# Kernel tuning notes

Measured on AMD Instinct MI355X. Metric: run time of the kernel, lower is better.

## Reference

```python
import jax, jax.numpy as jnp
import numpy as np

N = 50000      # nodes
E = 800000     # edges (before self loops)
IN = 128       # in_channels
C = 64         # out_channels per head
H = 4          # heads (both layers)
NEG_SLOPE = 0.2


def setup_inputs():
    key = jax.random.key(0)
    ks = jax.random.split(key, 14)
    nrm = lambda k, sh, s: jax.random.normal(k, sh, dtype=jnp.float32) * s
    x = nrm(ks[0], (N, IN), 1.0)
    edge_index = jax.random.randint(ks[1], (2, E), 0, N, dtype=jnp.int32)
    batch = jnp.zeros((N,), dtype=jnp.int32)
    edge_attr = jax.random.uniform(ks[2], (E, 1), dtype=jnp.float32)
    # layer 1 params (PyG GATConv: lin, att_src, att_dst, lin_edge, att_edge, bias)
    W1 = nrm(ks[3], (IN, H * C), 1.0 / np.sqrt(IN))
    We1 = nrm(ks[4], (1, H * C), 1.0)
    att_s1 = nrm(ks[5], (H, C), 1.0 / np.sqrt(C))
    att_d1 = nrm(ks[6], (H, C), 1.0 / np.sqrt(C))
    att_e1 = nrm(ks[7], (H, C), 1.0 / np.sqrt(C))
    b1 = jnp.zeros((H * C,), dtype=jnp.float32)
    # layer 2 params (in = H*C = 256)
    W2 = nrm(ks[8], (H * C, H * C), 1.0 / np.sqrt(H * C))
    We2 = nrm(ks[9], (1, H * C), 1.0)
    att_s2 = nrm(ks[10], (H, C), 1.0 / np.sqrt(C))
    att_d2 = nrm(ks[11], (H, C), 1.0 / np.sqrt(C))
    att_e2 = nrm(ks[12], (H, C), 1.0 / np.sqrt(C))
    b2 = jnp.zeros((H * C,), dtype=jnp.float32)
    return dict(x=x, edge_index=edge_index, batch=batch, edge_attr=edge_attr,
                W1=W1, We1=We1, att_s1=att_s1, att_d1=att_d1, att_e1=att_e1, b1=b1,
                W2=W2, We2=We2, att_s2=att_s2, att_d2=att_d2, att_e2=att_e2, b2=b2)


def gat_layer(h_in, src, dst, e_attr, W, We, att_s, att_d, att_e, b):
    n = h_in.shape[0]
    h = (h_in @ W).reshape(n, H, C)                      # [N,H,C]
    a_src = jnp.einsum('nhc,hc->nh', h, att_s)           # [N,H]
    a_dst = jnp.einsum('nhc,hc->nh', h, att_d)
    e = (e_attr @ We).reshape(-1, H, C)                  # [E',H,C]
    a_edge = jnp.einsum('ehc,hc->eh', e, att_e)          # [E',H]
    alpha = jax.nn.leaky_relu(a_src[src] + a_dst[dst] + a_edge, NEG_SLOPE)
    # softmax over edges grouped by destination node
    amax = jax.ops.segment_max(alpha, dst, num_segments=n)
    amax = jnp.where(jnp.isfinite(amax), amax, 0.0)
    ex = jnp.exp(alpha - amax[dst])
    denom = jax.ops.segment_sum(ex, dst, num_segments=n)
    a = ex / (denom[dst] + 1e-16)                        # [E',H]
    out = jax.ops.segment_sum(a[:, :, None] * h[src], dst, num_segments=n)
    return out.reshape(n, H * C) + b


def reference(x, edge_index, batch, edge_attr,
              W1, We1, att_s1, att_d1, att_e1, b1,
              W2, We2, att_s2, att_d2, att_e2, b2):
    n = x.shape[0]
    # PyG GATConv default: add self loops, self-loop edge_attr = mean fill
    loop = jnp.arange(n, dtype=edge_index.dtype)
    src = jnp.concatenate([edge_index[0], loop])
    dst = jnp.concatenate([edge_index[1], loop])
    ea_fill = jnp.broadcast_to(edge_attr.mean(axis=0, keepdims=True), (n, edge_attr.shape[1]))
    ea = jnp.concatenate([edge_attr, ea_fill], axis=0)
    h1 = gat_layer(x, src, dst, ea, W1, We1, att_s1, att_d1, att_e1, b1)
    h2 = gat_layer(h1, src, dst, ea, W2, We2, att_s2, att_d2, att_e2, b2)
    return h2
```

## Files before the change

### kernel.cpp

```cpp
#include <hip/hip_runtime.h>

#define NEG_SLOPE 0.2f

typedef __attribute__((ext_vector_type(8))) short bf16x8;
typedef __attribute__((ext_vector_type(4))) float f32x4;

__device__ inline unsigned short f2bf(float x) {
  unsigned int u = __float_as_uint(x);
  u += 0x7fffu + ((u >> 16) & 1u);
  return (unsigned short)(u >> 16);
}


__global__ void hist_kernel(const int* __restrict__ ei, int* __restrict__ counts,
                            int E, int Etot) {
  int e = blockIdx.x * blockDim.x + threadIdx.x;
  if (e >= Etot) return;
  int d = (e < E) ? ei[E + e] : (e - E);
  atomicAdd(&counts[d], 1);
}

__global__ void mean_kernel(const float* __restrict__ ea, float* __restrict__ acc, int E) {
  int i = blockIdx.x * blockDim.x + threadIdx.x;
  float s = 0.f;
  for (; i < E; i += gridDim.x * blockDim.x) s += ea[i];
#pragma unroll
  for (int off = 1; off < 64; off <<= 1) s += __shfl_xor(s, off, 64);
  if ((threadIdx.x & 63) == 0) atomicAdd(acc, s);
}

__global__ void scan_blocksum(const int* __restrict__ counts, int* __restrict__ bsum, int Nn) {
  int base = blockIdx.x * 4096 + threadIdx.x * 16;
  int s = 0;
#pragma unroll
  for (int i = 0; i < 16; i++) { int idx = base + i; if (idx < Nn) s += counts[idx]; }
#pragma unroll
  for (int off = 1; off < 64; off <<= 1) s += __shfl_xor(s, off, 64);
  __shared__ int ws_[4];
  if ((threadIdx.x & 63) == 0) ws_[threadIdx.x >> 6] = s;
  __syncthreads();
  if (threadIdx.x == 0) bsum[blockIdx.x] = ws_[0] + ws_[1] + ws_[2] + ws_[3];
}

__global__ void scan_offsets(int* bsum, int nb, int* rowptrN,
                             const float* meanacc, float* meanv, int E) {
  if (threadIdx.x == 0 && blockIdx.x == 0) {
    int acc = 0;
    for (int i = 0; i < nb; i++) { int v = bsum[i]; bsum[i] = acc; acc += v; }
    *rowptrN = acc;
    *meanv = *meanacc / (float)E;
  }
}

__global__ void scan_final(const int* __restrict__ counts, const int* __restrict__ bsum,
                           int* __restrict__ rowptr, int Nn) {
  int base = blockIdx.x * 4096 + threadIdx.x * 16;
  int v[16]; int s = 0;
#pragma unroll
  for (int i = 0; i < 16; i++) { int idx = base + i; v[i] = (idx < Nn) ? counts[idx] : 0; s += v[i]; }
  int lane = threadIdx.x & 63, wv = threadIdx.x >> 6;
  int incl = s;
#pragma unroll
  for (int off = 1; off < 64; off <<= 1) {
    int y = __shfl_up(incl, off, 64);
    if (lane >= off) incl += y;
  }
  __shared__ int wtot[4];
  if (lane == 63) wtot[wv] = incl;
  __syncthreads();
  int run = bsum[blockIdx.x] + incl - s;
  for (int i = 0; i < wv; i++) run += wtot[i];
  for (int i = 0; i < 16; i++) {
    int idx = base + i;
    if (idx < Nn) rowptr[idx] = run;
    run += v[i];
  }
}

__global__ void scatter_kernel(const int* __restrict__ ei, const float* __restrict__ eattr,
                               const float* __restrict__ meanv,
                               int* __restrict__ cursor, int2* __restrict__ epack,
                               int E, int Etot) {
  int e = blockIdx.x * blockDim.x + threadIdx.x;
  if (e >= Etot) return;
  int d, s; float ea;
  if (e < E) { d = ei[E + e]; s = ei[e]; ea = eattr[e]; }
  else       { d = e - E;     s = e - E; ea = meanv[0]; }
  int pos = atomicAdd(&cursor[d], 1);
  epack[pos] = make_int2(s, __float_as_int(ea));
}

__global__ void weatt_kernel(const float* __restrict__ We, const float* __restrict__ atte,
                             float* __restrict__ weatt) {
  int t = threadIdx.x;
  float p = We[t] * atte[t];
#pragma unroll
  for (int off = 1; off < 64; off <<= 1) p += __shfl_xor(p, off, 64);
  if ((t & 63) == 0) weatt[t >> 6] = p;
}

__global__ void wtrans_kernel(const float* __restrict__ W, unsigned short* __restrict__ Wt,
                              int K) {
  int t = blockIdx.x * blockDim.x + threadIdx.x;
  int n = t & 255, k = t >> 8;
  if (k >= K) return;
  Wt[(size_t)n * K + k] = f2bf(W[(size_t)k * 256 + n]);
}


template <int AF32>
__global__ __launch_bounds__(256) void gemm_att(const void* __restrict__ Ain,
                                                const unsigned short* __restrict__ Wt,
                                                unsigned short* __restrict__ Hb,
                                                const float* __restrict__ atts,
                                                const float* __restrict__ attd,
                                                float* __restrict__ asrc,
                                                float* __restrict__ adst,
                                                int M, int K) {
  __shared__ short As[32 * 64];
  __shared__ short Bs[256 * 64];
  const int tid = threadIdx.x;
  const int lane = tid & 63, wv = tid >> 6;
  const int l15 = lane & 15, l4 = lane >> 4;
  const int bm = blockIdx.x * 32;

  f32x4 acc[2][4] = {};

  for (int k0 = 0; k0 < K; k0 += 64) {
    {
      int r = tid >> 3, kc = (tid & 7) * 8;
      int gr = bm + r;
      bf16x8 v = {};
      if (gr < M) {
        if (AF32) {
          const float* src = (const float*)Ain + (size_t)gr * K + k0 + kc;
          float4 f0 = *(const float4*)src;
          float4 f1 = *(const float4*)(src + 4);
          v[0] = (short)f2bf(f0.x); v[1] = (short)f2bf(f0.y);
          v[2] = (short)f2bf(f0.z); v[3] = (short)f2bf(f0.w);
          v[4] = (short)f2bf(f1.x); v[5] = (short)f2bf(f1.y);
          v[6] = (short)f2bf(f1.z); v[7] = (short)f2bf(f1.w);
        } else {
          v = *(const bf16x8*)((const unsigned short*)Ain + (size_t)gr * K + k0 + kc);
        }
      }
      *(bf16x8*)&As[(r * 64 + kc) ^ ((r & 7) << 3)] = v;
    }
    {
      int c = tid & 7, nb = tid >> 3;
#pragma unroll
      for (int it = 0; it < 8; it++) {
        int n = nb + 32 * it;
        bf16x8 v = *(const bf16x8*)&Wt[(size_t)n * K + k0 + c * 8];
        *(bf16x8*)&Bs[(n * 64 + c * 8) ^ ((n & 7) << 3)] = v;
      }
    }
    __syncthreads();
    bf16x8 af[2][2], bfr[4][2];
#pragma unroll
    for (int rt = 0; rt < 2; rt++)
#pragma unroll
      for (int ks = 0; ks < 2; ks++) {
        int row = rt * 16 + l15;
        int kb = l4 * 8 + ks * 32;
        af[rt][ks] = *(const bf16x8*)&As[(row * 64 + kb) ^ ((row & 7) << 3)];
      }
#pragma unroll
    for (int ct = 0; ct < 4; ct++)
#pragma unroll
      for (int ks = 0; ks < 2; ks++) {
        int n = wv * 64 + ct * 16 + l15;
        int kb = l4 * 8 + ks * 32;
        bfr[ct][ks] = *(const bf16x8*)&Bs[(n * 64 + kb) ^ ((n & 7) << 3)];
      }
#pragma unroll
    for (int rt = 0; rt < 2; rt++)
#pragma unroll
      for (int ct = 0; ct < 4; ct++)
#pragma unroll
        for (int ks = 0; ks < 2; ks++)
          acc[rt][ct] = __builtin_amdgcn_mfma_f32_16x16x32_bf16(
              af[rt][ks], bfr[ct][ks], acc[rt][ct], 0, 0, 0);
    __syncthreads();
  }

  float s_att[4], d_att[4];
#pragma unroll
  for (int ct = 0; ct < 4; ct++) {
    s_att[ct] = atts[wv * 64 + ct * 16 + l15];
    d_att[ct] = attd[wv * 64 + ct * 16 + l15];
  }
  float ps[2][4] = {}, pd[2][4] = {};
#pragma unroll
  for (int rt = 0; rt < 2; rt++)
#pragma unroll
    for (int ct = 0; ct < 4; ct++)
#pragma unroll
      for (int i = 0; i < 4; i++) {
        float v = acc[rt][ct][i];
        int gr = bm + rt * 16 + l4 * 4 + i;
        if (gr < M) Hb[(size_t)gr * 256 + wv * 64 + ct * 16 + l15] = f2bf(v);
        ps[rt][i] = fmaf(v, s_att[ct], ps[rt][i]);
        pd[rt][i] = fmaf(v, d_att[ct], pd[rt][i]);
      }
#pragma unroll
  for (int rt = 0; rt < 2; rt++)
#pragma unroll
    for (int i = 0; i < 4; i++) {
#pragma unroll
      for (int off = 1; off < 16; off <<= 1) {
        ps[rt][i] += __shfl_xor(ps[rt][i], off, 64);
        pd[rt][i] += __shfl_xor(pd[rt][i], off, 64);
      }
    }
  if (l15 == 0) {
#pragma unroll
    for (int rt = 0; rt < 2; rt++)
#pragma unroll
      for (int i = 0; i < 4; i++) {
        int gr = bm + rt * 16 + l4 * 4 + i;
        if (gr < M) {
          asrc[gr * 4 + wv] = ps[rt][i];
          adst[gr * 4 + wv] = pd[rt][i];
        }
      }
  }
}


template <int OUTBF>
__global__ __launch_bounds__(256) void gat_agg(const unsigned short* __restrict__ Hb,
                                               const float* __restrict__ asrc,
                                               const float* __restrict__ adst,
                                               const int* __restrict__ rowptr,
                                               const int2* __restrict__ epack,
                                               const float* __restrict__ weatt,
                                               const float* __restrict__ bias,
                                               unsigned short* __restrict__ outb,
                                               float* __restrict__ outf, int Nn) {
  int wid = (blockIdx.x * blockDim.x + threadIdx.x) >> 6;
  int lane = threadIdx.x & 63;
  if (wid >= Nn) return;
  int beg = rowptr[wid], end = rowptr[wid + 1];
  int hh = lane >> 4;
  float wa = weatt[hh];
  float ad = adst[wid * 4 + hh];
  unsigned co = (unsigned)lane * 4u;

  float m0 = -1e30f, s0 = 0.f, m1 = -1e30f, s1 = 0.f;
  float4 a0 = {0.f, 0.f, 0.f, 0.f}, a1 = {0.f, 0.f, 0.f, 0.f};
  int p = beg;
  for (; p + 1 < end; p += 2) {
    int2 e0 = epack[p], e1 = epack[p + 1];
    float al0 = fmaf(__int_as_float(e0.y), wa, asrc[e0.x * 4 + hh] + ad);
    float al1 = fmaf(__int_as_float(e1.y), wa, asrc[e1.x * 4 + hh] + ad);
    al0 = al0 > 0.f ? al0 : al0 * NEG_SLOPE;
    al1 = al1 > 0.f ? al1 : al1 * NEG_SLOPE;
    uint2 hv0 = *(const uint2*)&Hb[(size_t)((unsigned)e0.x * 256u + co)];
    uint2 hv1 = *(const uint2*)&Hb[(size_t)((unsigned)e1.x * 256u + co)];
    float mn0 = fmaxf(m0, al0);
    float c0 = __expf(m0 - mn0);
    float w0 = __expf(al0 - mn0);
    m0 = mn0;
    s0 = fmaf(s0, c0, w0);
    a0.x = fmaf(a0.x, c0, w0 * __uint_as_float(hv0.x << 16));
    a0.y = fmaf(a0.y, c0, w0 * __uint_as_float(hv0.x & 0xffff0000u));
    a0.z = fmaf(a0.z, c0, w0 * __uint_as_float(hv0.y << 16));
    a0.w = fmaf(a0.w, c0, w0 * __uint_as_float(hv0.y & 0xffff0000u));
    float mn1 = fmaxf(m1, al1);
    float c1 = __expf(m1 - mn1);
    float w1 = __expf(al1 - mn1);
    m1 = mn1;
    s1 = fmaf(s1, c1, w1);
    a1.x = fmaf(a1.x, c1, w1 * __uint_as_float(hv1.x << 16));
    a1.y = fmaf(a1.y, c1, w1 * __uint_as_float(hv1.x & 0xffff0000u));
    a1.z = fmaf(a1.z, c1, w1 * __uint_as_float(hv1.y << 16));
    a1.w = fmaf(a1.w, c1, w1 * __uint_as_float(hv1.y & 0xffff0000u));
  }
  if (p < end) {
    int2 e0 = epack[p];
    float al0 = fmaf(__int_as_float(e0.y), wa, asrc[e0.x * 4 + hh] + ad);
    al0 = al0 > 0.f ? al0 : al0 * NEG_SLOPE;
    uint2 hv0 = *(const uint2*)&Hb[(size_t)((unsigned)e0.x * 256u + co)];
    float mn0 = fmaxf(m0, al0);
    float c0 = __expf(m0 - mn0);
    float w0 = __expf(al0 - mn0);
    m0 = mn0;
    s0 = fmaf(s0, c0, w0);
    a0.x = fmaf(a0.x, c0, w0 * __uint_as_float(hv0.x << 16));
    a0.y = fmaf(a0.y, c0, w0 * __uint_as_float(hv0.x & 0xffff0000u));
    a0.z = fmaf(a0.z, c0, w0 * __uint_as_float(hv0.y << 16));
    a0.w = fmaf(a0.w, c0, w0 * __uint_as_float(hv0.y & 0xffff0000u));
  }
  float mm = fmaxf(m0, m1);
  float c0 = __expf(m0 - mm), c1 = __expf(m1 - mm);
  float ssum = fmaf(s0, c0, s1 * c1);
  float inv = 1.f / (ssum + 1e-16f);
  float4 b4 = *(const float4*)&bias[co];
  float4 r;
  r.x = fmaf(fmaf(a0.x, c0, a1.x * c1), inv, b4.x);
  r.y = fmaf(fmaf(a0.y, c0, a1.y * c1), inv, b4.y);
  r.z = fmaf(fmaf(a0.z, c0, a1.z * c1), inv, b4.z);
  r.w = fmaf(fmaf(a0.w, c0, a1.w * c1), inv, b4.w);
  if (OUTBF) {
    unsigned lo = (unsigned)f2bf(r.x) | ((unsigned)f2bf(r.y) << 16);
    unsigned hi = (unsigned)f2bf(r.z) | ((unsigned)f2bf(r.w) << 16);
    *(uint2*)&outb[(size_t)wid * 256 + co] = make_uint2(lo, hi);
  } else {
    *(float4*)&outf[(size_t)wid * 256 + co] = r;
  }
}


extern "C" void kernel_launch(void* const* d_in, const int* in_sizes, int n_in,
                              void* d_out, int out_size, void* d_ws, size_t ws_size,
                              hipStream_t stream) {
  (void)n_in; (void)out_size; (void)ws_size;
  const float* x     = (const float*)d_in[0];
  const int*   ei    = (const int*)d_in[1];
  const float* eattr = (const float*)d_in[3];
  const float* W1    = (const float*)d_in[4];
  const float* We1   = (const float*)d_in[5];
  const float* atts1 = (const float*)d_in[6];
  const float* attd1 = (const float*)d_in[7];
  const float* atte1 = (const float*)d_in[8];
  const float* b1    = (const float*)d_in[9];
  const float* W2    = (const float*)d_in[10];
  const float* We2   = (const float*)d_in[11];
  const float* atts2 = (const float*)d_in[12];
  const float* attd2 = (const float*)d_in[13];
  const float* atte2 = (const float*)d_in[14];
  const float* b2    = (const float*)d_in[15];
  float* out = (float*)d_out;

  const int Nn   = in_sizes[0] / 128;
  const int E    = in_sizes[1] / 2;
  const int Etot = E + Nn;

  char* p = (char*)d_ws;
  auto alloc = [&](size_t bytes) { void* r = (void*)p; p += (bytes + 255) & ~(size_t)255; return r; };
  int*   rowptr  = (int*)alloc((size_t)(Nn + 1) * 4);
  int*   cursor  = (int*)alloc((size_t)Nn * 4);
  int*   counts  = (int*)alloc((size_t)Nn * 4);
  int2*  epack   = (int2*)alloc((size_t)Etot * 8);
  int*   bsum    = (int*)alloc(64 * 4);
  float* meanacc = (float*)alloc(4);
  float* meanv   = (float*)alloc(4);
  float* weatt1  = (float*)alloc(16);
  float* weatt2  = (float*)alloc(16);
  float* asrc    = (float*)alloc((size_t)Nn * 4 * 4);
  float* adst    = (float*)alloc((size_t)Nn * 4 * 4);
  unsigned short* hbuf = (unsigned short*)alloc((size_t)Nn * 256 * 2);
  unsigned short* h1b  = (unsigned short*)alloc((size_t)Nn * 256 * 2);
  unsigned short* Wt1  = (unsigned short*)alloc((size_t)256 * 128 * 2);
  unsigned short* Wt2  = (unsigned short*)alloc((size_t)256 * 256 * 2);

  const int NB = (Nn + 4095) / 4096;

  hipMemsetAsync(counts, 0, (size_t)Nn * 4, stream);
  hipMemsetAsync(meanacc, 0, 4, stream);

  hist_kernel<<<(Etot + 255) / 256, 256, 0, stream>>>(ei, counts, E, Etot);
  mean_kernel<<<512, 256, 0, stream>>>(eattr, meanacc, E);
  scan_blocksum<<<NB, 256, 0, stream>>>(counts, bsum, Nn);
  scan_offsets<<<1, 64, 0, stream>>>(bsum, NB, rowptr + Nn, meanacc, meanv, E);
  scan_final<<<NB, 256, 0, stream>>>(counts, bsum, rowptr, Nn);
  hipMemcpyAsync(cursor, rowptr, (size_t)Nn * 4, hipMemcpyDeviceToDevice, stream);
  scatter_kernel<<<(Etot + 255) / 256, 256, 0, stream>>>(ei, eattr, meanv, cursor, epack, E, Etot);
  weatt_kernel<<<1, 256, 0, stream>>>(We1, atte1, weatt1);
  weatt_kernel<<<1, 256, 0, stream>>>(We2, atte2, weatt2);
  wtrans_kernel<<<128, 256, 0, stream>>>(W1, Wt1, 128);
  wtrans_kernel<<<256, 256, 0, stream>>>(W2, Wt2, 256);

  const int gemmBlocks = (Nn + 31) / 32;
  const int nodeBlocks = (Nn + 3) / 4;

  gemm_att<1><<<gemmBlocks, 256, 0, stream>>>(x, Wt1, hbuf, atts1, attd1,
                                              asrc, adst, Nn, 128);
  gat_agg<1><<<nodeBlocks, 256, 0, stream>>>(hbuf, asrc, adst, rowptr, epack,
                                             weatt1, b1, h1b, nullptr, Nn);
  gemm_att<0><<<gemmBlocks, 256, 0, stream>>>(h1b, Wt2, hbuf, atts2, attd2,
                                              asrc, adst, Nn, 256);
  gat_agg<0><<<nodeBlocks, 256, 0, stream>>>(hbuf, asrc, adst, rowptr, epack,
                                             weatt2, b2, nullptr, out, Nn);
}
```

Measured before the change: 346.5 us.

## Replace online softmax with precomputed per-node upper-bound shift

The GEMM epilogue now tracks a global max of a_src per head through an order-preserving uint atomicMax. The aggregation kernel uses that max plus a_dst and the positive part of the edge weight as a fixed per-destination upper bound on the logits, so each edge needs one exp and plain accumulation instead of the online-softmax rescaling. Setup launches are also merged: one memset covers all zeroed buffers, scan_final writes cursor directly instead of a D2D copy, and the weatt and wtrans launches are fused. The fixed shift bound assumes edge_attr is in [0,1], and it can underflow if a node's true max is far below the global bound.

After: 459.0 us. 32.5% more time.

```diff
diff --git a/kernel.cpp b/kernel.cpp
--- a/kernel.cpp
+++ b/kernel.cpp
@@ -9,6 +9,15 @@
   unsigned int u = __float_as_uint(x);
   u += 0x7fffu + ((u >> 16) & 1u);
   return (unsigned short)(u >> 16);
+}
+
+__device__ inline unsigned fkey(float x) {
+  unsigned u = __float_as_uint(x);
+  return (u >> 31) ? ~u : (u | 0x80000000u);
+}
+__device__ inline float fkey_dec(unsigned k) {
+  unsigned u = (k & 0x80000000u) ? (k ^ 0x80000000u) : ~k;
+  return __uint_as_float(u);
 }
 
 
@@ -53,7 +62,7 @@
 }
 
 __global__ void scan_final(const int* __restrict__ counts, const int* __restrict__ bsum,
-                           int* __restrict__ rowptr, int Nn) {
+                           int* __restrict__ rowptr, int* __restrict__ cursor, int Nn) {
   int base = blockIdx.x * 4096 + threadIdx.x * 16;
   int v[16]; int s = 0;
 #pragma unroll
@@ -72,7 +81,7 @@
   for (int i = 0; i < wv; i++) run += wtot[i];
   for (int i = 0; i < 16; i++) {
     int idx = base + i;
-    if (idx < Nn) rowptr[idx] = run;
+    if (idx < Nn) { rowptr[idx] = run; cursor[idx] = run; }
     run += v[i];
   }
 }
@@ -90,18 +99,26 @@
   epack[pos] = make_int2(s, __float_as_int(ea));
 }
 
-__global__ void weatt_kernel(const float* __restrict__ We, const float* __restrict__ atte,
-                             float* __restrict__ weatt) {
+__global__ void weatt_kernel(const float* __restrict__ We1, const float* __restrict__ atte1,
+                             const float* __restrict__ We2, const float* __restrict__ atte2,
+                             float* __restrict__ weatt1, float* __restrict__ weatt2) {
   int t = threadIdx.x;
-  float p = We[t] * atte[t];
+  const float* We = (t < 256) ? We1 : We2;
+  const float* at = (t < 256) ? atte1 : atte2;
+  float* wo = (t < 256) ? weatt1 : weatt2;
+  int i = t & 255;
+  float p = We[i] * at[i];
 #pragma unroll
   for (int off = 1; off < 64; off <<= 1) p += __shfl_xor(p, off, 64);
-  if ((t & 63) == 0) weatt[t >> 6] = p;
-}
-
-__global__ void wtrans_kernel(const float* __restrict__ W, unsigned short* __restrict__ Wt,
-                              int K) {
-  int t = blockIdx.x * blockDim.x + threadIdx.x;
+  if ((i & 63) == 0) wo[i >> 6] = p;
+}
+
+__global__ void wtrans_kernel(const float* __restrict__ W1, unsigned short* __restrict__ Wt1,
+                              const float* __restrict__ W2, unsigned short* __restrict__ Wt2) {
+  int b = blockIdx.x;
+  const float* W; unsigned short* Wt; int K, t;
+  if (b < 128) { W = W1; Wt = Wt1; K = 128; t = b * 256 + threadIdx.x; }
+  else         { W = W2; Wt = Wt2; K = 256; t = (b - 128) * 256 + threadIdx.x; }
   int n = t & 255, k = t >> 8;
   if (k >= K) return;
   Wt[(size_t)n * K + k] = f2bf(W[(size_t)k * 256 + n]);
@@ -116,6 +133,7 @@
                                                 const float* __restrict__ attd,
                                                 float* __restrict__ asrc,
                                                 float* __restrict__ adst,
+                                                unsigned* __restrict__ gmaxk,
                                                 int M, int K) {
   __shared__ short As[32 * 64];
   __shared__ short Bs[256 * 64];
@@ -213,6 +231,14 @@
         pd[rt][i] += __shfl_xor(pd[rt][i], off, 64);
       }
     }
+  float mx = ps[0][0];
+#pragma unroll
+  for (int rt = 0; rt < 2; rt++)
+#pragma unroll
+    for (int i = 0; i < 4; i++) mx = fmaxf(mx, ps[rt][i]);
+  mx = fmaxf(mx, __shfl_xor(mx, 16, 64));
+  mx = fmaxf(mx, __shfl_xor(mx, 32, 64));
+  if (lane == 0) atomicMax(&gmaxk[wv], fkey(mx));
   if (l15 == 0) {
 #pragma unroll
     for (int rt = 0; rt < 2; rt++)
@@ -235,6 +261,7 @@
                                                const int* __restrict__ rowptr,
                                                const int2* __restrict__ epack,
                                                const float* __restrict__ weatt,
+                                               const unsigned* __restrict__ gmaxk,
                                                const float* __restrict__ bias,
                                                unsigned short* __restrict__ outb,
                                                float* __restrict__ outf, int Nn) {
@@ -245,63 +272,53 @@
   int hh = lane >> 4;
   float wa = weatt[hh];
   float ad = adst[wid * 4 + hh];
+  float braw = ad + fkey_dec(gmaxk[hh]) + fmaxf(wa, 0.f);
+  float b = fmaxf(braw, NEG_SLOPE * braw);
   unsigned co = (unsigned)lane * 4u;
 
-  float m0 = -1e30f, s0 = 0.f, m1 = -1e30f, s1 = 0.f;
+  float s0 = 0.f, s1 = 0.f;
   float4 a0 = {0.f, 0.f, 0.f, 0.f}, a1 = {0.f, 0.f, 0.f, 0.f};
   int p = beg;
   for (; p + 1 < end; p += 2) {
     int2 e0 = epack[p], e1 = epack[p + 1];
     float al0 = fmaf(__int_as_float(e0.y), wa, asrc[e0.x * 4 + hh] + ad);
     float al1 = fmaf(__int_as_float(e1.y), wa, asrc[e1.x * 4 + hh] + ad);
-    al0 = al0 > 0.f ? al0 : al0 * NEG_SLOPE;
-    al1 = al1 > 0.f ? al1 : al1 * NEG_SLOPE;
+    al0 = fmaxf(al0, NEG_SLOPE * al0);
+    al1 = fmaxf(al1, NEG_SLOPE * al1);
     uint2 hv0 = *(const uint2*)&Hb[(size_t)((unsigned)e0.x * 256u + co)];
     uint2 hv1 = *(const uint2*)&Hb[(size_t)((unsigned)e1.x * 256u + co)];
-    float mn0 = fmaxf(m0, al0);
-    float c0 = __expf(m0 - mn0);
-    float w0 = __expf(al0 - mn0);
-    m0 = mn0;
-    s0 = fmaf(s0, c0, w0);
-    a0.x = fmaf(a0.x, c0, w0 * __uint_as_float(hv0.x << 16));
-    a0.y = fmaf(a0.y, c0, w0 * __uint_as_float(hv0.x & 0xffff0000u));
-    a0.z = fmaf(a0.z, c0, w0 * __uint_as_float(hv0.y << 16));
-    a0.w = fmaf(a0.w, c0, w0 * __uint_as_float(hv0.y & 0xffff0000u));
-    float mn1 = fmaxf(m1, al1);
-    float c1 = __expf(m1 - mn1);
-    float w1 = __expf(al1 - mn1);
-    m1 = mn1;
-    s1 = fmaf(s1, c1, w1);
-    a1.x = fmaf(a1.x, c1, w1 * __uint_as_float(hv1.x << 16));
-    a1.y = fmaf(a1.y, c1, w1 * __uint_as_float(hv1.x & 0xffff0000u));
-    a1.z = fmaf(a1.z, c1, w1 * __uint_as_float(hv1.y << 16));
-    a1.w = fmaf(a1.w, c1, w1 * __uint_as_float(hv1.y & 0xffff0000u));
+    float w0 = __expf(al0 - b);
+    float w1 = __expf(al1 - b);
+    s0 += w0;
+    s1 += w1;
+    a0.x = fmaf(w0, __uint_as_float(hv0.x << 16), a0.x);
+    a0.y = fmaf(w0, __uint_as_float(hv0.x & 0xffff0000u), a0.y);
+    a0.z = fmaf(w0, __uint_as_float(hv0.y << 16), a0.z);
+    a0.w = fmaf(w0, __uint_as_float(hv0.y & 0xffff0000u), a0.w);
+    a1.x = fmaf(w1, __uint_as_float(hv1.x << 16), a1.x);
+    a1.y = fmaf(w1, __uint_as_float(hv1.x & 0xffff0000u), a1.y);
+    a1.z = fmaf(w1, __uint_as_float(hv1.y << 16), a1.z);
+    a1.w = fmaf(w1, __uint_as_float(hv1.y & 0xffff0000u), a1.w);
   }
   if (p < end) {
     int2 e0 = epack[p];
     float al0 = fmaf(__int_as_float(e0.y), wa, asrc[e0.x * 4 + hh] + ad);
-    al0 = al0 > 0.f ? al0 : al0 * NEG_SLOPE;
+    al0 = fmaxf(al0, NEG_SLOPE * al0);
     uint2 hv0 = *(const uint2*)&Hb[(size_t)((unsigned)e0.x * 256u + co)];
-    float mn0 = fmaxf(m0, al0);
-    float c0 = __expf(m0 - mn0);
-    float w0 = __expf(al0 - mn0);
-    m0 = mn0;
-    s0 = fmaf(s0, c0, w0);
-    a0.x = fmaf(a0.x, c0, w0 * __uint_as_float(hv0.x << 16));
-    a0.y = fmaf(a0.y, c0, w0 * __uint_as_float(hv0.x & 0xffff0000u));
-    a0.z = fmaf(a0.z, c0, w0 * __uint_as_float(hv0.y << 16));
-    a0.w = fmaf(a0.w, c0, w0 * __uint_as_float(hv0.y & 0xffff0000u));
-  }
-  float mm = fmaxf(m0, m1);
-  float c0 = __expf(m0 - mm), c1 = __expf(m1 - mm);
-  float ssum = fmaf(s0, c0, s1 * c1);
-  float inv = 1.f / (ssum + 1e-16f);
+    float w0 = __expf(al0 - b);
+    s0 += w0;
+    a0.x = fmaf(w0, __uint_as_float(hv0.x << 16), a0.x);
+    a0.y = fmaf(w0, __uint_as_float(hv0.x & 0xffff0000u), a0.y);
+    a0.z = fmaf(w0, __uint_as_float(hv0.y << 16), a0.z);
+    a0.w = fmaf(w0, __uint_as_float(hv0.y & 0xffff0000u), a0.w);
+  }
+  float inv = 1.f / (s0 + s1 + 1e-16f);
   float4 b4 = *(const float4*)&bias[co];
   float4 r;
-  r.x = fmaf(fmaf(a0.x, c0, a1.x * c1), inv, b4.x);
-  r.y = fmaf(fmaf(a0.y, c0, a1.y * c1), inv, b4.y);
-  r.z = fmaf(fmaf(a0.z, c0, a1.z * c1), inv, b4.z);
-  r.w = fmaf(fmaf(a0.w, c0, a1.w * c1), inv, b4.w);
+  r.x = fmaf(a0.x + a1.x, inv, b4.x);
+  r.y = fmaf(a0.y + a1.y, inv, b4.y);
+  r.z = fmaf(a0.z + a1.z, inv, b4.z);
+  r.w = fmaf(a0.w + a1.w, inv, b4.w);
   if (OUTBF) {
     unsigned lo = (unsigned)f2bf(r.x) | ((unsigned)f2bf(r.y) << 16);
     unsigned hi = (unsigned)f2bf(r.z) | ((unsigned)f2bf(r.w) << 16);
@@ -339,12 +356,15 @@
 
   char* p = (char*)d_ws;
   auto alloc = [&](size_t bytes) { void* r = (void*)p; p += (bytes + 255) & ~(size_t)255; return r; };
+  int*      counts  = (int*)alloc((size_t)Nn * 4);
+  float*    meanacc = (float*)alloc(4);
+  unsigned* gmaxk1  = (unsigned*)alloc(16);
+  unsigned* gmaxk2  = (unsigned*)alloc(16);
+  char* zero_end = p;
   int*   rowptr  = (int*)alloc((size_t)(Nn + 1) * 4);
   int*   cursor  = (int*)alloc((size_t)Nn * 4);
-  int*   counts  = (int*)alloc((size_t)Nn * 4);
   int2*  epack   = (int2*)alloc((size_t)Etot * 8);
   int*   bsum    = (int*)alloc(64 * 4);
-  float* meanacc = (float*)alloc(4);
   float* meanv   = (float*)alloc(4);
   float* weatt1  = (float*)alloc(16);
   float* weatt2  = (float*)alloc(16);
@@ -357,30 +377,26 @@
 
   const int NB = (Nn + 4095) / 4096;
 
-  hipMemsetAsync(counts, 0, (size_t)Nn * 4, stream);
-  hipMemsetAsync(meanacc, 0, 4, stream);
+  hipMemsetAsync(counts, 0, (size_t)(zero_end - (char*)counts), stream);
 
   hist_kernel<<<(Etot + 255) / 256, 256, 0, stream>>>(ei, counts, E, Etot);
   mean_kernel<<<512, 256, 0, stream>>>(eattr, meanacc, E);
   scan_blocksum<<<NB, 256, 0, stream>>>(counts, bsum, Nn);
   scan_offsets<<<1, 64, 0, stream>>>(bsum, NB, rowptr + Nn, meanacc, meanv, E);
-  scan_final<<<NB, 256, 0, stream>>>(counts, bsum, rowptr, Nn);
-  hipMemcpyAsync(cursor, rowptr, (size_t)Nn * 4, hipMemcpyDeviceToDevice, stream);
+  scan_final<<<NB, 256, 0, stream>>>(counts, bsum, rowptr, cursor, Nn);
   scatter_kernel<<<(Etot + 255) / 256, 256, 0, stream>>>(ei, eattr, meanv, cursor, epack, E, Etot);
-  weatt_kernel<<<1, 256, 0, stream>>>(We1, atte1, weatt1);
-  weatt_kernel<<<1, 256, 0, stream>>>(We2, atte2, weatt2);
-  wtrans_kernel<<<128, 256, 0, stream>>>(W1, Wt1, 128);
-  wtrans_kernel<<<256, 256, 0, stream>>>(W2, Wt2, 256);
+  weatt_kernel<<<1, 512, 0, stream>>>(We1, atte1, We2, atte2, weatt1, weatt2);
+  wtrans_kernel<<<384, 256, 0, stream>>>(W1, Wt1, W2, Wt2);
 
   const int gemmBlocks = (Nn + 31) / 32;
   const int nodeBlocks = (Nn + 3) / 4;
 
   gemm_att<1><<<gemmBlocks, 256, 0, stream>>>(x, Wt1, hbuf, atts1, attd1,
-                                              asrc, adst, Nn, 128);
+                                              asrc, adst, gmaxk1, Nn, 128);
   gat_agg<1><<<nodeBlocks, 256, 0, stream>>>(hbuf, asrc, adst, rowptr, epack,
-                                             weatt1, b1, h1b, nullptr, Nn);
+                                             weatt1, gmaxk1, b1, h1b, nullptr, Nn);
   gemm_att<0><<<gemmBlocks, 256, 0, stream>>>(h1b, Wt2, hbuf, atts2, attd2,
-                                              asrc, adst, Nn, 256);
+                                              asrc, adst, gmaxk2, Nn, 256);
   gat_agg<0><<<nodeBlocks, 256, 0, stream>>>(hbuf, asrc, adst, rowptr, epack,
-                                             weatt2, b2, nullptr, out, Nn);
-}
+                                             weatt2, gmaxk2, b2, nullptr, out, Nn);
+}
```
